# Kernel tuning notes

Measured on AMD Instinct MI355X. Metric: run time of the kernel, lower is better.

The kernel has to match this reference:

```python
import jax, jax.numpy as jnp
import numpy as np

HEADS = 16
DIM_HEAD = 64
QUERY_DIM = 1024
INNER = HEADS * DIM_HEAD  # 1024
SCALE = DIM_HEAD ** -0.5
B, T = 4, 2048


def setup_inputs() -> dict:
    key = jax.random.key(0)
    ks = jax.random.split(key, 7)
    s = 0.02
    return {
        "hidden_states": jax.random.normal(ks[0], (B, T, QUERY_DIM), dtype=jnp.float32),
        "attention_mask": jax.random.randint(ks[1], (B, T), 0, 2, dtype=jnp.int32),
        "Wq": jax.random.normal(ks[2], (QUERY_DIM, INNER), dtype=jnp.float32) * s,
        "Wk": jax.random.normal(ks[3], (QUERY_DIM, INNER), dtype=jnp.float32) * s,
        "Wv": jax.random.normal(ks[4], (QUERY_DIM, INNER), dtype=jnp.float32) * s,
        "Wo": jax.random.normal(ks[5], (INNER, QUERY_DIM), dtype=jnp.float32) * s,
        "bo": jnp.zeros((QUERY_DIM,), dtype=jnp.float32),
    }


def reference(hidden_states, attention_mask, Wq, Wk, Wv, Wo, bo):
    # QKV projections (bias=False)
    q = hidden_states @ Wq  # [B,T,INNER]
    k = hidden_states @ Wk
    v = hidden_states @ Wv
    # split heads: b t (h d) -> b h t d
    def split(x):
        b, t, _ = x.shape
        return x.reshape(b, t, HEADS, DIM_HEAD).transpose(0, 2, 1, 3)
    q, k, v = split(q), split(k), split(v)
    sim = jnp.einsum('bhid,bhjd->bhij', q, k) * SCALE  # [B,H,T,T]
    neg = jnp.finfo(sim.dtype).min
    mask = attention_mask[:, None, None, :]  # [B,1,1,T]
    sim = jnp.where(mask == 0, neg, sim)
    attn = jax.nn.softmax(sim, axis=-1)
    out = jnp.einsum('bhij,bhjd->bhid', attn, v)  # [B,H,T,D]
    out = out.transpose(0, 2, 1, 3).reshape(hidden_states.shape[0], hidden_states.shape[1], INNER)
    return out @ Wo + bo  # dropout p=0.0 -> identity
```

## Files before the change

kernel.cpp:

```cpp
#include <hip/hip_runtime.h>
#include <stdint.h>

typedef __attribute__((ext_vector_type(8))) __bf16 bf16x8;
typedef __attribute__((ext_vector_type(4))) float f32x4;

#define QSCALE 0.18033688011112042f

static __device__ __forceinline__ unsigned short f2bf(float x) {
  return __builtin_bit_cast(unsigned short, (__bf16)x);
}

static __device__ __forceinline__ void async16(const void* g, void* l) {
  __builtin_amdgcn_global_load_lds(
      (const __attribute__((address_space(1))) void*)g,
      (__attribute__((address_space(3))) void*)l, 16, 0, 0);
}

__global__ __launch_bounds__(256) void k_cvt(const float* __restrict__ x,
                                             unsigned short* __restrict__ y, int n4) {
  int i = blockIdx.x * 256 + threadIdx.x;
  if (i >= n4) return;
  float4 v = ((const float4*)x)[i];
  ushort4 o;
  o.x = f2bf(v.x); o.y = f2bf(v.y); o.z = f2bf(v.z); o.w = f2bf(v.w);
  ((ushort4*)y)[i] = o;
}

__global__ __launch_bounds__(256) void k_twt(const float* __restrict__ Wq,
                                             const float* __restrict__ Wk,
                                             const float* __restrict__ Wv,
                                             const float* __restrict__ Wo,
                                             unsigned short* __restrict__ wt_qkv,
                                             unsigned short* __restrict__ wot) {
  __shared__ float tile[64][65];
  const int mat = blockIdx.z;
  const float* W = (mat == 0) ? Wq : (mat == 1) ? Wk : (mat == 2) ? Wv : Wo;
  const float scale = (mat == 0) ? QSCALE : 1.0f;
  const int k0 = blockIdx.y * 64, n0 = blockIdx.x * 64;
  const int t = threadIdx.x, c = t & 63;
#pragma unroll
  for (int j = 0; j < 16; ++j) {
    int r = j * 4 + (t >> 6);
    tile[r][c] = W[(size_t)(k0 + r) * 1024 + n0 + c] * scale;
  }
  __syncthreads();
  unsigned short* dst = (mat < 3) ? (wt_qkv + (size_t)mat * 1024 * 1024) : wot;
#pragma unroll
  for (int j = 0; j < 16; ++j) {
    int nr = j * 4 + (t >> 6);
    dst[(size_t)(n0 + nr) * 1024 + k0 + c] = f2bf(tile[c][nr]);
  }
}

__global__ __launch_bounds__(256) void k_gemm_qkv(const unsigned short* __restrict__ A,
                                                  const unsigned short* __restrict__ Bt,
                                                  unsigned short* __restrict__ q_lin,
                                                  unsigned short* __restrict__ k_lin,
                                                  unsigned short* __restrict__ vT) {
  __shared__ __align__(16) unsigned short aT[2][128 * 32];
  __shared__ __align__(16) unsigned short bT[2][128 * 32];
  const int tid = threadIdx.x, lane = tid & 63, w = tid >> 6;
  const int wr = w >> 1, wc = w & 1;
  const int m0 = blockIdx.y * 128, n0 = blockIdx.x * 128;
  const char* Ab = (const char*)A;
  const char* Bb = (const char*)Bt;
  char* aTb = (char*)aT; char* bTb = (char*)bT;
  f32x4 acc[4][4] = {};

  const int ci0 = w * 2, bo0 = ci0 * 1024 + lane * 16;
  const int srow0 = bo0 >> 6, scol0 = bo0 & 63;
#define G_STAGE(buf, kt)                                                              \
  {                                                                                   \
    _Pragma("unroll")                                                                 \
    for (int j = 0; j < 2; ++j) {                                                     \
      const int row = srow0 + j * 16;                                                 \
      async16(Ab + ((size_t)(m0 + row) * 1024 + (kt) * 32) * 2 + scol0,               \
              aTb + (buf) * 8192 + (ci0 + j) * 1024);                                 \
      async16(Bb + ((size_t)(n0 + row) * 1024 + (kt) * 32) * 2 + scol0,               \
              bTb + (buf) * 8192 + (ci0 + j) * 1024);                                 \
    }                                                                                 \
  }

  G_STAGE(0, 0);
  __syncthreads();
  for (int kt = 0; kt < 32; ++kt) {
    const int cur = kt & 1;
    if (kt + 1 < 32) G_STAGE(cur ^ 1, kt + 1);
    bf16x8 af[4], bfr[4];
#pragma unroll
    for (int mi = 0; mi < 4; ++mi)
      af[mi] = *(const bf16x8*)(aTb + cur * 8192 +
               ((wr * 64 + mi * 16 + (lane & 15)) * 32 + (lane >> 4) * 8) * 2);
#pragma unroll
    for (int ni = 0; ni < 4; ++ni)
      bfr[ni] = *(const bf16x8*)(bTb + cur * 8192 +
               ((wc * 64 + ni * 16 + (lane & 15)) * 32 + (lane >> 4) * 8) * 2);
#pragma unroll
    for (int mi = 0; mi < 4; ++mi)
#pragma unroll
      for (int ni = 0; ni < 4; ++ni)
        acc[mi][ni] = __builtin_amdgcn_mfma_f32_16x16x32_bf16(af[mi], bfr[ni], acc[mi][ni], 0, 0, 0);
    __syncthreads();
  }
#undef G_STAGE

  const int mat = n0 >> 10;
  const int nn0 = n0 & 1023;
  if (mat < 2) {
    unsigned short* dst = (mat == 0) ? q_lin : k_lin;
#pragma unroll
    for (int mi = 0; mi < 4; ++mi) {
      const int r0 = m0 + wr * 64 + mi * 16 + (lane >> 4) * 4;
#pragma unroll
      for (int ni = 0; ni < 4; ++ni) {
        const int c = nn0 + wc * 64 + ni * 16 + (lane & 15);
#pragma unroll
        for (int r = 0; r < 4; ++r)
          dst[(size_t)(r0 + r) * 1024 + c] = f2bf(acc[mi][ni][r]);
      }
    }
  } else {
#pragma unroll
    for (int mi = 0; mi < 4; ++mi) {
      const int r0 = m0 + wr * 64 + mi * 16 + (lane >> 4) * 4;
      const int b = r0 >> 11, tt = r0 & 2047;
#pragma unroll
      for (int ni = 0; ni < 4; ++ni) {
        const int c = nn0 + wc * 64 + ni * 16 + (lane & 15);
        const int h = c >> 6, d = c & 63;
        ushort4 o;
        o.x = f2bf(acc[mi][ni][0]); o.y = f2bf(acc[mi][ni][1]);
        o.z = f2bf(acc[mi][ni][2]); o.w = f2bf(acc[mi][ni][3]);
        *(ushort4*)(vT + ((size_t)((b * 16 + h) * 64 + d) << 11) + tt) = o;
      }
    }
  }
}

__global__ __launch_bounds__(256, 3) void k_attn(const unsigned short* __restrict__ q_lin,
                                                 const unsigned short* __restrict__ k_lin,
                                                 const unsigned short* __restrict__ vT,
                                                 const int* __restrict__ mask,
                                                 unsigned short* __restrict__ o_lin) {
  __shared__ __align__(16) unsigned short Kt[2][64 * 64];
  __shared__ __align__(16) unsigned short Vt[2][64 * 64];
  __shared__ __align__(16) unsigned short Pl[4][16 * 64];
  __shared__ __align__(16) float biasl[2][64];
  const int tid = threadIdx.x, lane = tid & 63, w = tid >> 6;
  const int qq = lane & 15, g = lane >> 4;
  const int bh = blockIdx.y, b = bh >> 4, h = bh & 15;
  const int t0 = blockIdx.x * 128;
  const char* qbp = (const char*)(q_lin + (size_t)b * 2048 * 1024 + h * 64);
  const char* kbp = (const char*)(k_lin + (size_t)b * 2048 * 1024 + h * 64);
  const char* vbp = (const char*)(vT + ((size_t)bh * 64 << 11));
  unsigned short* obp = o_lin + (size_t)b * 2048 * 1024 + h * 64;
  const int* mp = mask + b * 2048;
  char* KtB = (char*)Kt; char* VtB = (char*)Vt;
  char* PlB = (char*)(&Pl[w][0]);
  const int psw = (qq & 7) << 4;

  bf16x8 qf[2][2];
#pragma unroll
  for (int qb = 0; qb < 2; ++qb)
#pragma unroll
    for (int dc = 0; dc < 2; ++dc)
      qf[qb][dc] = *(const bf16x8*)(qbp +
          ((size_t)(t0 + w * 32 + qb * 16 + qq) * 1024 + dc * 32 + g * 8) * 2);

  f32x4 oacc[2][4] = {};
  float m_[2] = {-3.0e38f, -3.0e38f}, l_[2] = {0.f, 0.f};

  const int sci = w * 2, sbo = sci * 1024 + lane * 16;
  const int srow = sbo >> 7;
  const int scolb = (sbo & 127) ^ ((srow & 7) << 4);
#define A_STAGE(buf, kv0)                                                             \
  {                                                                                   \
    _Pragma("unroll")                                                                 \
    for (int j = 0; j < 2; ++j) {                                                     \
      const int row = srow + j * 8;                                                   \
      async16(kbp + (size_t)((kv0) + row) * 2048 + scolb,                             \
              KtB + (buf) * 8192 + (sci + j) * 1024);                                 \
      async16(vbp + (size_t)row * 4096 + (size_t)(kv0) * 2 + scolb,                   \
              VtB + (buf) * 8192 + (sci + j) * 1024);                                 \
    }                                                                                 \
    if (tid < 64) biasl[buf][tid] = (mp[(kv0) + tid] == 0) ? -__builtin_inff() : 0.0f;\
  }

  A_STAGE(0, 0);
  __syncthreads();

  for (int kt = 0; kt < 32; ++kt) {
    const int cur = kt & 1;
    if (kt + 1 < 32) A_STAGE(cur ^ 1, (kt + 1) * 64);

    bf16x8 kf[4][2], vf[4][2];
#pragma unroll
    for (int kb = 0; kb < 4; ++kb)
#pragma unroll
      for (int dc = 0; dc < 2; ++dc) {
        const int row = kb * 16 + qq;
        kf[kb][dc] = *(const bf16x8*)(KtB + cur * 8192 + row * 128 +
                                      ((dc * 64 + g * 16) ^ ((row & 7) << 4)));
      }
#pragma unroll
    for (int db = 0; db < 4; ++db)
#pragma unroll
      for (int hc = 0; hc < 2; ++hc) {
        const int row = db * 16 + qq;
        vf[db][hc] = *(const bf16x8*)(VtB + cur * 8192 + row * 128 +
                                      ((hc * 64 + g * 16) ^ ((row & 7) << 4)));
      }
    float4 bb[4];
#pragma unroll
    for (int kb = 0; kb < 4; ++kb) bb[kb] = ((const float4*)biasl[cur])[kb * 4 + g];

#pragma unroll
    for (int qb = 0; qb < 2; ++qb) {
      f32x4 s[4];
#pragma unroll
      for (int kb = 0; kb < 4; ++kb) {
        f32x4 sc = {};
        sc = __builtin_amdgcn_mfma_f32_16x16x32_bf16(kf[kb][0], qf[qb][0], sc, 0, 0, 0);
        sc = __builtin_amdgcn_mfma_f32_16x16x32_bf16(kf[kb][1], qf[qb][1], sc, 0, 0, 0);
        sc[0] += bb[kb].x; sc[1] += bb[kb].y; sc[2] += bb[kb].z; sc[3] += bb[kb].w;
        s[kb] = sc;
      }
      float mx[4];
#pragma unroll
      for (int kb = 0; kb < 4; ++kb)
        mx[kb] = fmaxf(fmaxf(s[kb][0], s[kb][1]), fmaxf(s[kb][2], s[kb][3]));
      float mt = fmaxf(fmaxf(mx[0], mx[1]), fmaxf(mx[2], mx[3]));
      mt = fmaxf(mt, __shfl_xor(mt, 16));
      mt = fmaxf(mt, __shfl_xor(mt, 32));
      if (__any(mt > m_[qb] + 8.0f)) {
        const float mn = fmaxf(m_[qb], mt);
        const float sf = __builtin_amdgcn_exp2f(m_[qb] - mn);
        m_[qb] = mn;
        l_[qb] *= sf;
#pragma unroll
        for (int db = 0; db < 4; ++db)
#pragma unroll
          for (int r = 0; r < 4; ++r) oacc[qb][db][r] *= sf;
      }
      const float mm = m_[qb];
      float rs = 0.f;
#pragma unroll
      for (int kb = 0; kb < 4; ++kb) {
        const float e0 = __builtin_amdgcn_exp2f(s[kb][0] - mm);
        const float e1 = __builtin_amdgcn_exp2f(s[kb][1] - mm);
        const float e2 = __builtin_amdgcn_exp2f(s[kb][2] - mm);
        const float e3 = __builtin_amdgcn_exp2f(s[kb][3] - mm);
        rs += (e0 + e1) + (e2 + e3);
        ushort4 pk;
        pk.x = f2bf(e0); pk.y = f2bf(e1); pk.z = f2bf(e2); pk.w = f2bf(e3);
        *(ushort4*)(PlB + qq * 128 + ((kb * 32 + g * 8) ^ psw)) = pk;
      }
      rs += __shfl_xor(rs, 16);
      rs += __shfl_xor(rs, 32);
      l_[qb] += rs;
      bf16x8 pf[2];
#pragma unroll
      for (int hc = 0; hc < 2; ++hc)
        pf[hc] = *(const bf16x8*)(PlB + qq * 128 + ((hc * 64 + g * 16) ^ psw));
#pragma unroll
      for (int db = 0; db < 4; ++db) {
        oacc[qb][db] = __builtin_amdgcn_mfma_f32_16x16x32_bf16(vf[db][0], pf[0], oacc[qb][db], 0, 0, 0);
        oacc[qb][db] = __builtin_amdgcn_mfma_f32_16x16x32_bf16(vf[db][1], pf[1], oacc[qb][db], 0, 0, 0);
      }
    }
    __syncthreads();
  }
#undef A_STAGE

#pragma unroll
  for (int qb = 0; qb < 2; ++qb) {
    const float inv = 1.0f / l_[qb];
    const int qrow = t0 + w * 32 + qb * 16 + qq;
#pragma unroll
    for (int db = 0; db < 4; ++db) {
      ushort4 o;
      o.x = f2bf(oacc[qb][db][0] * inv); o.y = f2bf(oacc[qb][db][1] * inv);
      o.z = f2bf(oacc[qb][db][2] * inv); o.w = f2bf(oacc[qb][db][3] * inv);
      *(ushort4*)(obp + (size_t)qrow * 1024 + db * 16 + g * 4) = o;
    }
  }
}

__global__ __launch_bounds__(256) void k_gemm_out(const unsigned short* __restrict__ A,
                                                  const unsigned short* __restrict__ Bt,
                                                  const float* __restrict__ bias,
                                                  float* __restrict__ out) {
  __shared__ __align__(16) unsigned short aT[2][128 * 32];
  __shared__ __align__(16) unsigned short bT[2][128 * 32];
  const int tid = threadIdx.x, lane = tid & 63, w = tid >> 6;
  const int wr = w >> 1, wc = w & 1;
  const int m0 = blockIdx.y * 128, n0 = blockIdx.x * 128;
  const char* Ab = (const char*)A;
  const char* Bb = (const char*)Bt;
  char* aTb = (char*)aT; char* bTb = (char*)bT;
  f32x4 acc[4][4] = {};

  const int ci0 = w * 2, bo0 = ci0 * 1024 + lane * 16;
  const int srow0 = bo0 >> 6, scol0 = bo0 & 63;
#define G_STAGE(buf, kt)                                                              \
  {                                                                                   \
    _Pragma("unroll")                                                                 \
    for (int j = 0; j < 2; ++j) {                                                     \
      const int row = srow0 + j * 16;                                                 \
      async16(Ab + ((size_t)(m0 + row) * 1024 + (kt) * 32) * 2 + scol0,               \
              aTb + (buf) * 8192 + (ci0 + j) * 1024);                                 \
      async16(Bb + ((size_t)(n0 + row) * 1024 + (kt) * 32) * 2 + scol0,               \
              bTb + (buf) * 8192 + (ci0 + j) * 1024);                                 \
    }                                                                                 \
  }

  G_STAGE(0, 0);
  __syncthreads();
  for (int kt = 0; kt < 32; ++kt) {
    const int cur = kt & 1;
    if (kt + 1 < 32) G_STAGE(cur ^ 1, kt + 1);
    bf16x8 af[4], bfr[4];
#pragma unroll
    for (int mi = 0; mi < 4; ++mi)
      af[mi] = *(const bf16x8*)(aTb + cur * 8192 +
               ((wr * 64 + mi * 16 + (lane & 15)) * 32 + (lane >> 4) * 8) * 2);
#pragma unroll
    for (int ni = 0; ni < 4; ++ni)
      bfr[ni] = *(const bf16x8*)(bTb + cur * 8192 +
               ((wc * 64 + ni * 16 + (lane & 15)) * 32 + (lane >> 4) * 8) * 2);
#pragma unroll
    for (int mi = 0; mi < 4; ++mi)
#pragma unroll
      for (int ni = 0; ni < 4; ++ni)
        acc[mi][ni] = __builtin_amdgcn_mfma_f32_16x16x32_bf16(af[mi], bfr[ni], acc[mi][ni], 0, 0, 0);
    __syncthreads();
  }
#undef G_STAGE
#pragma unroll
  for (int mi = 0; mi < 4; ++mi) {
    const int r0 = m0 + wr * 64 + mi * 16 + (lane >> 4) * 4;
#pragma unroll
    for (int ni = 0; ni < 4; ++ni) {
      const int c = n0 + wc * 64 + ni * 16 + (lane & 15);
      const float bb = bias[c];
#pragma unroll
      for (int r = 0; r < 4; ++r)
        out[(size_t)(r0 + r) * 1024 + c] = acc[mi][ni][r] + bb;
    }
  }
}

extern "C" void kernel_launch(void* const* d_in, const int* in_sizes, int n_in,
                              void* d_out, int out_size, void* d_ws, size_t ws_size,
                              hipStream_t stream) {
  const float* hs   = (const float*)d_in[0];
  const int*   mask = (const int*)d_in[1];
  const float* Wq   = (const float*)d_in[2];
  const float* Wk   = (const float*)d_in[3];
  const float* Wv   = (const float*)d_in[4];
  const float* Wo   = (const float*)d_in[5];
  const float* bo   = (const float*)d_in[6];
  float* out = (float*)d_out;

  const size_t MB = 1024 * 1024;
  char* ws = (char*)d_ws;
  unsigned short* hs_bf  = (unsigned short*)(ws);
  unsigned short* wt_qkv = (unsigned short*)(ws + 16 * MB);
  unsigned short* wot    = (unsigned short*)(ws + 22 * MB);
  unsigned short* q_lin  = (unsigned short*)(ws + 24 * MB);
  unsigned short* k_lin  = (unsigned short*)(ws + 40 * MB);
  unsigned short* vT     = (unsigned short*)(ws + 56 * MB);
  unsigned short* o_lin  = (unsigned short*)(ws + 72 * MB);

  k_cvt<<<8192, 256, 0, stream>>>(hs, hs_bf, 2097152);
  k_twt<<<dim3(16, 16, 4), 256, 0, stream>>>(Wq, Wk, Wv, Wo, wt_qkv, wot);
  k_gemm_qkv<<<dim3(24, 64), 256, 0, stream>>>(hs_bf, wt_qkv, q_lin, k_lin, vT);
  k_attn<<<dim3(16, 64), 256, 0, stream>>>(q_lin, k_lin, vT, mask, o_lin);
  k_gemm_out<<<dim3(8, 64), 256, 0, stream>>>(o_lin, wot, bo, out);
}
```

Measured before the change: 352.2 us.

## Use 32x32 MFMA in attention, merge prep kernels, remap block order for XCDs

Rewrites the attention inner loop so each wave computes scores and PV with 32x32x16 bf16 MFMAs over 32 query rows, and adds s_setprio around the MFMA sections. The two conversion kernels are merged into a single prep launch. All three GEMM/attention kernels remap the block index so consecutive blocks land on the same XCD, aiming for better L2 reuse. The aim is fewer MFMA issues, less LDS traffic and one fewer launch, at the cost of more register pressure in the attention kernel.

```diff
diff --git a/kernel.cpp b/kernel.cpp
--- a/kernel.cpp
+++ b/kernel.cpp
@@ -3,40 +3,46 @@
 
 typedef __attribute__((ext_vector_type(8))) __bf16 bf16x8;
 typedef __attribute__((ext_vector_type(4))) float f32x4;
+typedef __attribute__((ext_vector_type(16))) float f32x16;
 
 #define QSCALE 0.18033688011112042f
 
 static __device__ __forceinline__ unsigned short f2bf(float x) {
   return __builtin_bit_cast(unsigned short, (__bf16)x);
 }
-
+static __device__ __forceinline__ unsigned pkbf(float a, float b) {
+  union { unsigned short h[2]; unsigned u; } r;
+  r.h[0] = f2bf(a); r.h[1] = f2bf(b); return r.u;
+}
 static __device__ __forceinline__ void async16(const void* g, void* l) {
   __builtin_amdgcn_global_load_lds(
       (const __attribute__((address_space(1))) void*)g,
       (__attribute__((address_space(3))) void*)l, 16, 0, 0);
 }
 
-__global__ __launch_bounds__(256) void k_cvt(const float* __restrict__ x,
-                                             unsigned short* __restrict__ y, int n4) {
-  int i = blockIdx.x * 256 + threadIdx.x;
-  if (i >= n4) return;
-  float4 v = ((const float4*)x)[i];
-  ushort4 o;
-  o.x = f2bf(v.x); o.y = f2bf(v.y); o.z = f2bf(v.z); o.w = f2bf(v.w);
-  ((ushort4*)y)[i] = o;
-}
-
-__global__ __launch_bounds__(256) void k_twt(const float* __restrict__ Wq,
-                                             const float* __restrict__ Wk,
-                                             const float* __restrict__ Wv,
-                                             const float* __restrict__ Wo,
-                                             unsigned short* __restrict__ wt_qkv,
-                                             unsigned short* __restrict__ wot) {
+__global__ __launch_bounds__(256) void k_prep(const float* __restrict__ hs,
+                                              const float* __restrict__ Wq,
+                                              const float* __restrict__ Wk,
+                                              const float* __restrict__ Wv,
+                                              const float* __restrict__ Wo,
+                                              unsigned short* __restrict__ hs_bf,
+                                              unsigned short* __restrict__ wt_qkv,
+                                              unsigned short* __restrict__ wot) {
   __shared__ float tile[64][65];
-  const int mat = blockIdx.z;
+  const int bid = blockIdx.x;
+  if (bid < 8192) {
+    const int i = bid * 256 + threadIdx.x;
+    float4 v = ((const float4*)hs)[i];
+    ushort4 o;
+    o.x = f2bf(v.x); o.y = f2bf(v.y); o.z = f2bf(v.z); o.w = f2bf(v.w);
+    ((ushort4*)hs_bf)[i] = o;
+    return;
+  }
+  const int idx = bid - 8192;
+  const int mat = idx >> 8;
   const float* W = (mat == 0) ? Wq : (mat == 1) ? Wk : (mat == 2) ? Wv : Wo;
   const float scale = (mat == 0) ? QSCALE : 1.0f;
-  const int k0 = blockIdx.y * 64, n0 = blockIdx.x * 64;
+  const int n0 = (idx & 15) * 64, k0 = ((idx >> 4) & 15) * 64;
   const int t = threadIdx.x, c = t & 63;
 #pragma unroll
   for (int j = 0; j < 16; ++j) {
@@ -61,7 +67,9 @@
   __shared__ __align__(16) unsigned short bT[2][128 * 32];
   const int tid = threadIdx.x, lane = tid & 63, w = tid >> 6;
   const int wr = w >> 1, wc = w & 1;
-  const int m0 = blockIdx.y * 128, n0 = blockIdx.x * 128;
+  int flat = blockIdx.y * 24 + blockIdx.x;
+  flat = (flat & 7) * 192 + (flat >> 3);
+  const int m0 = (flat / 24) * 128, n0 = (flat % 24) * 128;
   const char* Ab = (const char*)A;
   const char* Bb = (const char*)Bt;
   char* aTb = (char*)aT; char* bTb = (char*)bT;
@@ -144,31 +152,33 @@
                                                  unsigned short* __restrict__ o_lin) {
   __shared__ __align__(16) unsigned short Kt[2][64 * 64];
   __shared__ __align__(16) unsigned short Vt[2][64 * 64];
-  __shared__ __align__(16) unsigned short Pl[4][16 * 64];
+  __shared__ __align__(16) unsigned short Pl[4][32 * 64];
   __shared__ __align__(16) float biasl[2][64];
   const int tid = threadIdx.x, lane = tid & 63, w = tid >> 6;
-  const int qq = lane & 15, g = lane >> 4;
-  const int bh = blockIdx.y, b = bh >> 4, h = bh & 15;
-  const int t0 = blockIdx.x * 128;
-  const char* qbp = (const char*)(q_lin + (size_t)b * 2048 * 1024 + h * 64);
-  const char* kbp = (const char*)(k_lin + (size_t)b * 2048 * 1024 + h * 64);
-  const char* vbp = (const char*)(vT + ((size_t)bh * 64 << 11));
+  const int qi = lane & 31, hi = lane >> 5;
+  int flat = blockIdx.y * 16 + blockIdx.x;
+  flat = (flat & 7) * 128 + (flat >> 3);
+  const int bh = flat >> 4, b = bh >> 4, h = bh & 15;
+  const int t0 = (flat & 15) * 128;
+  const unsigned short* qbp = q_lin + (size_t)b * 2048 * 1024 + h * 64;
+  const unsigned short* kbp = k_lin + (size_t)b * 2048 * 1024 + h * 64;
+  const unsigned short* vbp = vT + ((size_t)bh * 64 << 11);
   unsigned short* obp = o_lin + (size_t)b * 2048 * 1024 + h * 64;
   const int* mp = mask + b * 2048;
   char* KtB = (char*)Kt; char* VtB = (char*)Vt;
   char* PlB = (char*)(&Pl[w][0]);
-  const int psw = (qq & 7) << 4;
-
-  bf16x8 qf[2][2];
-#pragma unroll
-  for (int qb = 0; qb < 2; ++qb)
-#pragma unroll
-    for (int dc = 0; dc < 2; ++dc)
-      qf[qb][dc] = *(const bf16x8*)(qbp +
-          ((size_t)(t0 + w * 32 + qb * 16 + qq) * 1024 + dc * 32 + g * 8) * 2);
-
-  f32x4 oacc[2][4] = {};
-  float m_[2] = {-3.0e38f, -3.0e38f}, l_[2] = {0.f, 0.f};
+  const int rsw = (qi & 7) << 4;
+
+  bf16x8 qf[4];
+  {
+    const unsigned short* qrow = qbp + (size_t)(t0 + w * 32 + qi) * 1024;
+#pragma unroll
+    for (int s = 0; s < 4; ++s)
+      qf[s] = *(const bf16x8*)(qrow + s * 16 + hi * 8);
+  }
+
+  f32x16 oaccA = {}, oaccB = {};
+  float m_ = -3.0e38f, l_ = 0.f;
 
   const int sci = w * 2, sbo = sci * 1024 + lane * 16;
   const int srow = sbo >> 7;
@@ -178,9 +188,9 @@
     _Pragma("unroll")                                                                 \
     for (int j = 0; j < 2; ++j) {                                                     \
       const int row = srow + j * 8;                                                   \
-      async16(kbp + (size_t)((kv0) + row) * 2048 + scolb,                             \
+      async16(kbp + (size_t)((kv0) + row) * 1024 + (scolb >> 1),                      \
               KtB + (buf) * 8192 + (sci + j) * 1024);                                 \
-      async16(vbp + (size_t)row * 4096 + (size_t)(kv0) * 2 + scolb,                   \
+      async16(vbp + (size_t)row * 2048 + (kv0) + (scolb >> 1),                        \
               VtB + (buf) * 8192 + (sci + j) * 1024);                                 \
     }                                                                                 \
     if (tid < 64) biasl[buf][tid] = (mp[(kv0) + tid] == 0) ? -__builtin_inff() : 0.0f;\
@@ -193,96 +203,103 @@
     const int cur = kt & 1;
     if (kt + 1 < 32) A_STAGE(cur ^ 1, (kt + 1) * 64);
 
-    bf16x8 kf[4][2], vf[4][2];
-#pragma unroll
-    for (int kb = 0; kb < 4; ++kb)
-#pragma unroll
-      for (int dc = 0; dc < 2; ++dc) {
-        const int row = kb * 16 + qq;
-        kf[kb][dc] = *(const bf16x8*)(KtB + cur * 8192 + row * 128 +
-                                      ((dc * 64 + g * 16) ^ ((row & 7) << 4)));
-      }
-#pragma unroll
-    for (int db = 0; db < 4; ++db)
-#pragma unroll
-      for (int hc = 0; hc < 2; ++hc) {
-        const int row = db * 16 + qq;
-        vf[db][hc] = *(const bf16x8*)(VtB + cur * 8192 + row * 128 +
-                                      ((hc * 64 + g * 16) ^ ((row & 7) << 4)));
-      }
-    float4 bb[4];
-#pragma unroll
-    for (int kb = 0; kb < 4; ++kb) bb[kb] = ((const float4*)biasl[cur])[kb * 4 + g];
-
-#pragma unroll
-    for (int qb = 0; qb < 2; ++qb) {
-      f32x4 s[4];
-#pragma unroll
-      for (int kb = 0; kb < 4; ++kb) {
-        f32x4 sc = {};
-        sc = __builtin_amdgcn_mfma_f32_16x16x32_bf16(kf[kb][0], qf[qb][0], sc, 0, 0, 0);
-        sc = __builtin_amdgcn_mfma_f32_16x16x32_bf16(kf[kb][1], qf[qb][1], sc, 0, 0, 0);
-        sc[0] += bb[kb].x; sc[1] += bb[kb].y; sc[2] += bb[kb].z; sc[3] += bb[kb].w;
-        s[kb] = sc;
-      }
-      float mx[4];
-#pragma unroll
-      for (int kb = 0; kb < 4; ++kb)
-        mx[kb] = fmaxf(fmaxf(s[kb][0], s[kb][1]), fmaxf(s[kb][2], s[kb][3]));
-      float mt = fmaxf(fmaxf(mx[0], mx[1]), fmaxf(mx[2], mx[3]));
-      mt = fmaxf(mt, __shfl_xor(mt, 16));
-      mt = fmaxf(mt, __shfl_xor(mt, 32));
-      if (__any(mt > m_[qb] + 8.0f)) {
-        const float mn = fmaxf(m_[qb], mt);
-        const float sf = __builtin_amdgcn_exp2f(m_[qb] - mn);
-        m_[qb] = mn;
-        l_[qb] *= sf;
-#pragma unroll
-        for (int db = 0; db < 4; ++db)
-#pragma unroll
-          for (int r = 0; r < 4; ++r) oacc[qb][db][r] *= sf;
-      }
-      const float mm = m_[qb];
-      float rs = 0.f;
-#pragma unroll
-      for (int kb = 0; kb < 4; ++kb) {
-        const float e0 = __builtin_amdgcn_exp2f(s[kb][0] - mm);
-        const float e1 = __builtin_amdgcn_exp2f(s[kb][1] - mm);
-        const float e2 = __builtin_amdgcn_exp2f(s[kb][2] - mm);
-        const float e3 = __builtin_amdgcn_exp2f(s[kb][3] - mm);
-        rs += (e0 + e1) + (e2 + e3);
-        ushort4 pk;
-        pk.x = f2bf(e0); pk.y = f2bf(e1); pk.z = f2bf(e2); pk.w = f2bf(e3);
-        *(ushort4*)(PlB + qq * 128 + ((kb * 32 + g * 8) ^ psw)) = pk;
-      }
-      rs += __shfl_xor(rs, 16);
-      rs += __shfl_xor(rs, 32);
-      l_[qb] += rs;
-      bf16x8 pf[2];
-#pragma unroll
-      for (int hc = 0; hc < 2; ++hc)
-        pf[hc] = *(const bf16x8*)(PlB + qq * 128 + ((hc * 64 + g * 16) ^ psw));
-#pragma unroll
-      for (int db = 0; db < 4; ++db) {
-        oacc[qb][db] = __builtin_amdgcn_mfma_f32_16x16x32_bf16(vf[db][0], pf[0], oacc[qb][db], 0, 0, 0);
-        oacc[qb][db] = __builtin_amdgcn_mfma_f32_16x16x32_bf16(vf[db][1], pf[1], oacc[qb][db], 0, 0, 0);
-      }
-    }
+    f32x16 sA = {}, sB = {};
+    __builtin_amdgcn_s_setprio(1);
+#pragma unroll
+    for (int s = 0; s < 4; ++s) {
+      bf16x8 kf = *(const bf16x8*)(KtB + cur * 8192 + (qi)*128 + ((s * 32 + hi * 16) ^ rsw));
+      sA = __builtin_amdgcn_mfma_f32_32x32x16_bf16(kf, qf[s], sA, 0, 0, 0);
+    }
+#pragma unroll
+    for (int s = 0; s < 4; ++s) {
+      bf16x8 kf = *(const bf16x8*)(KtB + cur * 8192 + (32 + qi) * 128 + ((s * 32 + hi * 16) ^ rsw));
+      sB = __builtin_amdgcn_mfma_f32_32x32x16_bf16(kf, qf[s], sB, 0, 0, 0);
+    }
+    __builtin_amdgcn_s_setprio(0);
+
+    float e[32];
+#pragma unroll
+    for (int u = 0; u < 4; ++u) {
+      const float4 b4 = ((const float4*)biasl[cur])[2 * u + hi];
+      e[4 * u + 0] = sA[4 * u + 0] + b4.x; e[4 * u + 1] = sA[4 * u + 1] + b4.y;
+      e[4 * u + 2] = sA[4 * u + 2] + b4.z; e[4 * u + 3] = sA[4 * u + 3] + b4.w;
+    }
+#pragma unroll
+    for (int u = 0; u < 4; ++u) {
+      const float4 b4 = ((const float4*)biasl[cur])[8 + 2 * u + hi];
+      e[16 + 4 * u + 0] = sB[4 * u + 0] + b4.x; e[16 + 4 * u + 1] = sB[4 * u + 1] + b4.y;
+      e[16 + 4 * u + 2] = sB[4 * u + 2] + b4.z; e[16 + 4 * u + 3] = sB[4 * u + 3] + b4.w;
+    }
+
+    float t16[16];
+#pragma unroll
+    for (int i = 0; i < 16; ++i) t16[i] = fmaxf(e[i], e[16 + i]);
+#pragma unroll
+    for (int i = 0; i < 8; ++i) t16[i] = fmaxf(t16[i], t16[8 + i]);
+#pragma unroll
+    for (int i = 0; i < 4; ++i) t16[i] = fmaxf(t16[i], t16[4 + i]);
+    float mt = fmaxf(fmaxf(t16[0], t16[1]), fmaxf(t16[2], t16[3]));
+    mt = fmaxf(mt, __shfl_xor(mt, 32));
+
+    if (__any(mt > m_ + 8.0f)) {
+      const float mn = fmaxf(m_, mt);
+      const float sf = __builtin_amdgcn_exp2f(m_ - mn);
+      m_ = mn; l_ *= sf;
+#pragma unroll
+      for (int r = 0; r < 16; ++r) { oaccA[r] *= sf; oaccB[r] *= sf; }
+    }
+
+#pragma unroll
+    for (int i = 0; i < 32; ++i) e[i] = __builtin_amdgcn_exp2f(e[i] - m_);
+    float u16[16];
+#pragma unroll
+    for (int i = 0; i < 16; ++i) u16[i] = e[i] + e[16 + i];
+#pragma unroll
+    for (int i = 0; i < 8; ++i) u16[i] += u16[8 + i];
+#pragma unroll
+    for (int i = 0; i < 4; ++i) u16[i] += u16[4 + i];
+    float rs = (u16[0] + u16[1]) + (u16[2] + u16[3]);
+    l_ += rs + __shfl_xor(rs, 32);
+
+#pragma unroll
+    for (int u = 0; u < 8; ++u) {
+      uint2 pk;
+      pk.x = pkbf(e[4 * u + 0], e[4 * u + 1]);
+      pk.y = pkbf(e[4 * u + 2], e[4 * u + 3]);
+      *(uint2*)(PlB + qi * 128 + ((16 * u + 8 * hi) ^ rsw)) = pk;
+    }
+    bf16x8 pw[4];
+#pragma unroll
+    for (int t = 0; t < 4; ++t)
+      pw[t] = *(const bf16x8*)(PlB + qi * 128 + ((32 * t + 16 * hi) ^ rsw));
+
+    __builtin_amdgcn_s_setprio(1);
+#pragma unroll
+    for (int t = 0; t < 4; ++t) {
+      bf16x8 vf = *(const bf16x8*)(VtB + cur * 8192 + (qi)*128 + ((t * 32 + hi * 16) ^ rsw));
+      oaccA = __builtin_amdgcn_mfma_f32_32x32x16_bf16(vf, pw[t], oaccA, 0, 0, 0);
+    }
+#pragma unroll
+    for (int t = 0; t < 4; ++t) {
+      bf16x8 vf = *(const bf16x8*)(VtB + cur * 8192 + (32 + qi) * 128 + ((t * 32 + hi * 16) ^ rsw));
+      oaccB = __builtin_amdgcn_mfma_f32_32x32x16_bf16(vf, pw[t], oaccB, 0, 0, 0);
+    }
+    __builtin_amdgcn_s_setprio(0);
     __syncthreads();
   }
 #undef A_STAGE
 
-#pragma unroll
-  for (int qb = 0; qb < 2; ++qb) {
-    const float inv = 1.0f / l_[qb];
-    const int qrow = t0 + w * 32 + qb * 16 + qq;
-#pragma unroll
-    for (int db = 0; db < 4; ++db) {
-      ushort4 o;
-      o.x = f2bf(oacc[qb][db][0] * inv); o.y = f2bf(oacc[qb][db][1] * inv);
-      o.z = f2bf(oacc[qb][db][2] * inv); o.w = f2bf(oacc[qb][db][3] * inv);
-      *(ushort4*)(obp + (size_t)qrow * 1024 + db * 16 + g * 4) = o;
-    }
+  const float inv = 1.0f / l_;
+  unsigned short* orow = obp + (size_t)(t0 + w * 32 + qi) * 1024;
+#pragma unroll
+  for (int u = 0; u < 4; ++u) {
+    ushort4 oa, ob;
+    oa.x = f2bf(oaccA[4 * u + 0] * inv); oa.y = f2bf(oaccA[4 * u + 1] * inv);
+    oa.z = f2bf(oaccA[4 * u + 2] * inv); oa.w = f2bf(oaccA[4 * u + 3] * inv);
+    ob.x = f2bf(oaccB[4 * u + 0] * inv); ob.y = f2bf(oaccB[4 * u + 1] * inv);
+    ob.z = f2bf(oaccB[4 * u + 2] * inv); ob.w = f2bf(oaccB[4 * u + 3] * inv);
+    *(ushort4*)(orow + 8 * u + 4 * hi) = oa;
+    *(ushort4*)(orow + 32 + 8 * u + 4 * hi) = ob;
   }
 }
 
@@ -294,7 +311,9 @@
   __shared__ __align__(16) unsigned short bT[2][128 * 32];
   const int tid = threadIdx.x, lane = tid & 63, w = tid >> 6;
   const int wr = w >> 1, wc = w & 1;
-  const int m0 = blockIdx.y * 128, n0 = blockIdx.x * 128;
+  int flat = blockIdx.y * 8 + blockIdx.x;
+  flat = (flat & 7) * 64 + (flat >> 3);
+  const int m0 = (flat >> 3) * 128, n0 = (flat & 7) * 128;
   const char* Ab = (const char*)A;
   const char* Bb = (const char*)Bt;
   char* aTb = (char*)aT; char* bTb = (char*)bT;
@@ -372,8 +391,7 @@
   unsigned short* vT     = (unsigned short*)(ws + 56 * MB);
   unsigned short* o_lin  = (unsigned short*)(ws + 72 * MB);
 
-  k_cvt<<<8192, 256, 0, stream>>>(hs, hs_bf, 2097152);
-  k_twt<<<dim3(16, 16, 4), 256, 0, stream>>>(Wq, Wk, Wv, Wo, wt_qkv, wot);
+  k_prep<<<9216, 256, 0, stream>>>(hs, Wq, Wk, Wv, Wo, hs_bf, wt_qkv, wot);
   k_gemm_qkv<<<dim3(24, 64), 256, 0, stream>>>(hs_bf, wt_qkv, q_lin, k_lin, vT);
   k_attn<<<dim3(16, 64), 256, 0, stream>>>(q_lin, k_lin, vT, mask, o_lin);
   k_gemm_out<<<dim3(8, 64), 256, 0, stream>>>(o_lin, wot, bo, out);
```

After: 315.9 us. 10.3% less time.
